# Kernel optimization log

Measured on AMD Instinct MI355X. Metric: run time of the kernel, lower is better.

## Reference

```python
import jax, jax.numpy as jnp
import numpy as np

DIM = 1024
DIM_HEAD = 64
HEADS = 16
DIM_INNER = DIM_HEAD * HEADS  # 1024


def setup_inputs() -> dict:
    key = jax.random.key(0)
    k1, k2, k3 = jax.random.split(key, 3)
    b, n = 2, 2048
    x = jax.random.normal(k1, (b, n, DIM), dtype=jnp.float32)
    gamma = jnp.ones((DIM,), dtype=jnp.float32)
    # torch Linear weight [out,in] applied as x @ W.T; store pre-transposed [in,out]
    w_qkv = jax.random.normal(k2, (DIM, 3 * DIM_INNER), dtype=jnp.float32) * (DIM ** -0.5)
    w_out = jax.random.normal(k3, (DIM_INNER, DIM), dtype=jnp.float32) * (DIM_INNER ** -0.5)
    return {"x": x, "gamma": gamma, "w_qkv": w_qkv, "w_out": w_out}


def reference(x, gamma, w_qkv, w_out):
    h, d = HEADS, DIM_HEAD
    scale = d ** -0.5
    rms_scale = DIM ** 0.5
    # RMSNorm: F.normalize(x, dim=-1) * sqrt(dim) * gamma  (eps=1e-12 clamp on L2 norm)
    norm = jnp.maximum(jnp.linalg.norm(x, axis=-1, keepdims=True), 1e-12)
    xn = x / norm * rms_scale * gamma
    b, n, _ = x.shape
    qkv = xn @ w_qkv  # [b, n, 3*h*d]
    qkv = qkv.reshape(b, n, 3, h, d)
    q = qkv[:, :, 0].transpose(0, 2, 1, 3) * scale  # [b, h, n, d]
    k = qkv[:, :, 1].transpose(0, 2, 1, 3)
    v = qkv[:, :, 2].transpose(0, 2, 1, 3)
    sim = jnp.einsum('bhid,bhjd->bhij', q, k)  # [b, h, n, n]
    causal_mask = jnp.triu(jnp.ones((n, n), dtype=bool), k=1)
    neg = -jnp.finfo(sim.dtype).max
    sim = jnp.where(causal_mask, neg, sim)
    attn = jax.nn.softmax(sim, axis=-1)
    out = jnp.einsum('bhij,bhjd->bhid', attn, v)  # [b, h, n, d]
    out = out.transpose(0, 2, 1, 3).reshape(b, n, h * d)
    return out @ w_out
```

## Files before the change

### kernel.cpp

```cpp
#include <hip/hip_runtime.h>
#include <hip/hip_bf16.h>

typedef __bf16 bf16x8 __attribute__((ext_vector_type(8)));
typedef short s16x4 __attribute__((ext_vector_type(4)));
typedef short s16x8 __attribute__((ext_vector_type(8)));
typedef float f32x4 __attribute__((ext_vector_type(4)));
typedef unsigned short u16x8 __attribute__((ext_vector_type(8)));

#define MFMA_K32(a, b, c) __builtin_amdgcn_mfma_f32_16x16x32_bf16(a, b, c, 0, 0, 0)

static __device__ __forceinline__ f32x4 mfma_k16(s16x4 a, s16x4 b, f32x4 c) {
#ifdef __HIP_DEVICE_COMPILE__
    return __builtin_amdgcn_mfma_f32_16x16x16bf16_1k(a, b, c, 0, 0, 0);
#else
    return c;
#endif
}

static __device__ __forceinline__ float fast_exp2(float x) {
#ifdef __HIP_DEVICE_COMPILE__
    return __builtin_amdgcn_exp2f(x);
#else
    return x;
#endif
}

#define GLL16(gp, lp)                                              \
    __builtin_amdgcn_global_load_lds(                              \
        (const __attribute__((address_space(1))) void*)(gp),       \
        (__attribute__((address_space(3))) void*)(lp), 16, 0, 0)

static __device__ __forceinline__ unsigned short f2bf(float f) {
    unsigned int u = __float_as_uint(f);
    u += 0x7fffu + ((u >> 16) & 1u);
    return (unsigned short)(u >> 16);
}

static __device__ __forceinline__ unsigned int cvtpk_bf16(float lo, float hi) {
#if defined(__HIP_DEVICE_COMPILE__) && __has_builtin(__builtin_amdgcn_cvt_pk_bf16_f32)
    typedef __bf16 bf16x2 __attribute__((ext_vector_type(2)));
    bf16x2 r = __builtin_amdgcn_cvt_pk_bf16_f32(lo, hi);
    return __builtin_bit_cast(unsigned int, r);
#else
    return (unsigned int)f2bf(lo) | ((unsigned int)f2bf(hi) << 16);
#endif
}

#define LOG2E 1.44269504088896340736f

__global__ __launch_bounds__(256) void prep_k(
    const float* __restrict__ x, const float* __restrict__ gamma,
    const float* __restrict__ w_qkv, const float* __restrict__ w_out,
    unsigned short* __restrict__ xn, unsigned short* __restrict__ wtq,
    unsigned short* __restrict__ wto) {
    __shared__ float sm[32][33];
    int bid = blockIdx.x, tid = threadIdx.x;
    if (bid < 4096) {
        const float* in;
        unsigned short* out;
        int R = 1024, C, bx, by;
        if (bid < 3072) { in = w_qkv; out = wtq; C = 3072; bx = bid % 96; by = bid / 96; }
        else { int b2 = bid - 3072; in = w_out; out = wto; C = 1024; bx = b2 % 32; by = b2 / 32; }
        int c0 = bx * 32, r0 = by * 32;
        int tr = tid >> 5, tc = tid & 31;
#pragma unroll
        for (int i = 0; i < 4; i++)
            sm[tr + i * 8][tc] = in[(size_t)(r0 + tr + i * 8) * C + c0 + tc];
        __syncthreads();
#pragma unroll
        for (int i = 0; i < 4; i++)
            out[(size_t)(c0 + tr + i * 8) * R + r0 + tc] = f2bf(sm[tc][tr + i * 8]);
    } else {
        int row = bid - 4096;
        const float* xr = x + (size_t)row * 1024;
        float4 v = *(const float4*)(xr + tid * 4);
        float ss = v.x * v.x + v.y * v.y + v.z * v.z + v.w * v.w;
#pragma unroll
        for (int off = 1; off < 64; off <<= 1) ss += __shfl_xor(ss, off, 64);
        if ((tid & 63) == 0) sm[0][tid >> 6] = ss;
        __syncthreads();
        float tot = sm[0][0] + sm[0][1] + sm[0][2] + sm[0][3];
        float f = 32.0f / fmaxf(sqrtf(tot), 1e-12f);
        float4 g = *(const float4*)(gamma + tid * 4);
        uint2 o;
        o.x = cvtpk_bf16(v.x * f * g.x, v.y * f * g.y);
        o.y = cvtpk_bf16(v.z * f * g.z, v.w * f * g.w);
        *(uint2*)(xn + (size_t)row * 1024 + tid * 4) = o;
    }
}

template <int MODE, int BM>
__global__ __launch_bounds__(256) void gemm_bt_k(
    const unsigned short* __restrict__ A, const unsigned short* __restrict__ BT,
    float* __restrict__ C, unsigned short* __restrict__ qw,
    unsigned short* __restrict__ kw, unsigned short* __restrict__ vw,
    int M, int N, int K) {
    constexpr int RT = 4;
    constexpr int CT = (BM == 128) ? 4 : 2;
    __shared__ unsigned short As[BM][32];
    __shared__ unsigned short Bs[128][32];
    int tid = threadIdx.x;
    int wave = tid >> 6, lane = tid & 63, quad = lane >> 4, l16 = lane & 15;
    int wrb, wcb;
    if constexpr (BM == 128) { wrb = (wave >> 1) * 64; wcb = (wave & 1) * 64; }
    else { wrb = 0; wcb = wave * 32; }
    int m0 = blockIdx.y * BM, n0 = blockIdx.x * 128;
    int lrow = lane >> 2, lcol = (lane & 3) * 8;
    const unsigned short *Ag0, *Ag1 = nullptr;
    if constexpr (BM == 128) {
        Ag0 = A + (size_t)(m0 + wave * 32 + lrow) * K + lcol;
        Ag1 = A + (size_t)(m0 + wave * 32 + 16 + lrow) * K + lcol;
    } else {
        Ag0 = A + (size_t)(m0 + wave * 16 + lrow) * K + lcol;
    }
    const unsigned short* Bg0 = BT + (size_t)(n0 + wave * 32 + lrow) * K + lcol;
    const unsigned short* Bg1 = BT + (size_t)(n0 + wave * 32 + 16 + lrow) * K + lcol;
    f32x4 acc[RT][CT] = {};
    for (int k0 = 0; k0 < K; k0 += 32) {
        __syncthreads();
        if constexpr (BM == 128) {
            GLL16(Ag0 + k0, &As[wave * 32][0]);
            GLL16(Ag1 + k0, &As[wave * 32 + 16][0]);
        } else {
            GLL16(Ag0 + k0, &As[wave * 16][0]);
        }
        GLL16(Bg0 + k0, &Bs[wave * 32][0]);
        GLL16(Bg1 + k0, &Bs[wave * 32 + 16][0]);
        __syncthreads();
        bf16x8 af[RT], bfr[CT];
#pragma unroll
        for (int t = 0; t < RT; t++)
            af[t] = *(const bf16x8*)&As[wrb + t * 16 + l16][quad * 8];
#pragma unroll
        for (int t = 0; t < CT; t++)
            bfr[t] = *(const bf16x8*)&Bs[wcb + t * 16 + l16][quad * 8];
#pragma unroll
        for (int rt = 0; rt < RT; rt++)
#pragma unroll
            for (int ct = 0; ct < CT; ct++)
                acc[rt][ct] = MFMA_K32(af[rt], bfr[ct], acc[rt][ct]);
    }
#pragma unroll
    for (int rt = 0; rt < RT; rt++) {
        int mb = m0 + wrb + rt * 16 + quad * 4;
        int b = mb >> 11, nn = mb & 2047;
#pragma unroll
        for (int ct = 0; ct < CT; ct++) {
            int col = n0 + wcb + ct * 16 + l16;
            if (MODE == 0) {
#pragma unroll
                for (int r = 0; r < 4; r++)
                    C[(size_t)(mb + r) * N + col] = acc[rt][ct][r];
            } else {
                int sec = col >> 10, ci = col & 1023;
                int hh = ci >> 6, dd = ci & 63;
                int bh = b * 16 + hh;
                if (sec == 0) {
#pragma unroll
                    for (int r = 0; r < 4; r++)
                        qw[((size_t)bh * 2048 + nn + r) * 64 + dd] =
                            f2bf(acc[rt][ct][r] * (0.125f * LOG2E));
                } else if (sec == 1) {
#pragma unroll
                    for (int r = 0; r < 4; r++)
                        kw[((size_t)bh * 2048 + nn + r) * 64 + dd] = f2bf(acc[rt][ct][r]);
                } else {
                    uint2 pk;
                    pk.x = cvtpk_bf16(acc[rt][ct][0], acc[rt][ct][1]);
                    pk.y = cvtpk_bf16(acc[rt][ct][2], acc[rt][ct][3]);
                    int sb = (nn & ~63) | (((nn >> 2) & 3) << 4) | (((nn >> 4) & 3) << 2);
                    *(uint2*)&vw[((size_t)bh * 64 + dd) * 2048 + sb] = pk;
                }
            }
        }
    }
}

__global__ __launch_bounds__(256) void attn_k(
    const unsigned short* __restrict__ q, const unsigned short* __restrict__ k,
    const unsigned short* __restrict__ vt, unsigned short* __restrict__ o) {
    __shared__ unsigned short Ks[2][128][72];
    __shared__ unsigned short Vt[2][64][136];
    int bh = blockIdx.x;
    int qt = 31 - (int)blockIdx.y;
    int tid = threadIdx.x, wave = tid >> 6, lane = tid & 63;
    int quad = lane >> 4, l16 = lane & 15;
    int b = bh >> 4, h = bh & 15;
    const unsigned short* qg = q + (size_t)bh * 2048 * 64;
    const unsigned short* kg = k + (size_t)bh * 2048 * 64;
    const unsigned short* vg = vt + (size_t)bh * 64 * 2048;
    int krow = tid >> 1, kcol = (tid & 1) * 32;
    int vrow = tid >> 2, vcol = (tid & 3) * 32;
    int q0w = qt * 64 + wave * 16;
    bf16x8 bq[2];
#pragma unroll
    for (int ks = 0; ks < 2; ks++)
        bq[ks] = *(const bf16x8*)&qg[(size_t)(q0w + l16) * 64 + ks * 32 + quad * 8];
    f32x4 ot[4] = {};
    float mrun = -1e38f, lrun = 0.f;
    int nkt = (qt >> 1) + 1;
    u16x8 pk[4], pv[4];
    {
        const unsigned short* kp = kg + (size_t)krow * 64 + kcol;
        const unsigned short* vp = vg + (size_t)vrow * 2048 + vcol;
#pragma unroll
        for (int i = 0; i < 4; i++) {
            pk[i] = *(const u16x8*)(kp + i * 8);
            pv[i] = *(const u16x8*)(vp + i * 8);
        }
#pragma unroll
        for (int i = 0; i < 4; i++) {
            *(u16x8*)&Ks[0][krow][kcol + i * 8] = pk[i];
            *(u16x8*)&Vt[0][vrow][vcol + i * 8] = pv[i];
        }
    }
    __syncthreads();
    for (int kt = 0; kt < nkt; kt++) {
        int cb = kt & 1;
        bool pf = (kt + 1 < nkt);
        if (pf) {
            const unsigned short* kp = kg + (size_t)((kt + 1) * 128 + krow) * 64 + kcol;
            const unsigned short* vp = vg + (size_t)vrow * 2048 + (kt + 1) * 128 + vcol;
#pragma unroll
            for (int i = 0; i < 4; i++) {
                pk[i] = *(const u16x8*)(kp + i * 8);
                pv[i] = *(const u16x8*)(vp + i * 8);
            }
        }
        f32x4 sf[8];
#pragma unroll
        for (int ct = 0; ct < 8; ct++) {
            bf16x8 ak0 = *(const bf16x8*)&Ks[cb][ct * 16 + l16][quad * 8];
            bf16x8 ak1 = *(const bf16x8*)&Ks[cb][ct * 16 + l16][32 + quad * 8];
            f32x4 s = {};
            s = MFMA_K32(ak0, bq[0], s);
            s = MFMA_K32(ak1, bq[1], s);
            sf[ct] = s;
        }
        if (kt == nkt - 1) {
            int qrow = q0w + l16;
            int keyb = kt * 128 + quad * 4;
#pragma unroll
            for (int ct = 0; ct < 8; ct++)
#pragma unroll
                for (int r = 0; r < 4; r++)
                    if (keyb + ct * 16 + r > qrow) sf[ct][r] = -1e30f;
        }
        float mx = -1e30f;
#pragma unroll
        for (int ct = 0; ct < 8; ct++)
#pragma unroll
            for (int r = 0; r < 4; r++) mx = fmaxf(mx, sf[ct][r]);
        mx = fmaxf(mx, __shfl_xor(mx, 16, 64));
        mx = fmaxf(mx, __shfl_xor(mx, 32, 64));
        float mnew = fmaxf(mrun, mx);
        float al = fast_exp2(mrun - mnew);
        mrun = mnew;
        float rs = 0.f;
#pragma unroll
        for (int ct = 0; ct < 8; ct++)
#pragma unroll
            for (int r = 0; r < 4; r++) {
                float p = fast_exp2(sf[ct][r] - mnew);
                sf[ct][r] = p;
                rs += p;
            }
        rs += __shfl_xor(rs, 16, 64);
        rs += __shfl_xor(rs, 32, 64);
        lrun = lrun * al + rs;
        s16x4 bpr[8];
#pragma unroll
        for (int ct = 0; ct < 8; ct++) {
            uint2 u;
            u.x = cvtpk_bf16(sf[ct][0], sf[ct][1]);
            u.y = cvtpk_bf16(sf[ct][2], sf[ct][3]);
            bpr[ct] = __builtin_bit_cast(s16x4, u);
        }
        if (__any(al < 1.0f)) {
#pragma unroll
            for (int dt = 0; dt < 4; dt++)
#pragma unroll
                for (int r = 0; r < 4; r++) ot[dt][r] *= al;
        }
#pragma unroll
        for (int dt = 0; dt < 4; dt++) {
#pragma unroll
            for (int blk = 0; blk < 2; blk++)
#pragma unroll
                for (int p = 0; p < 2; p++) {
                    s16x8 av = *(const s16x8*)&Vt[cb][dt * 16 + l16]
                                                  [blk * 64 + quad * 16 + p * 8];
                    s16x4 lo = __builtin_shufflevector(av, av, 0, 1, 2, 3);
                    s16x4 hi = __builtin_shufflevector(av, av, 4, 5, 6, 7);
                    int ct = blk * 4 + p * 2;
                    ot[dt] = mfma_k16(lo, bpr[ct], ot[dt]);
                    ot[dt] = mfma_k16(hi, bpr[ct + 1], ot[dt]);
                }
        }
        if (pf) {
#pragma unroll
            for (int i = 0; i < 4; i++) {
                *(u16x8*)&Ks[1 - cb][krow][kcol + i * 8] = pk[i];
                *(u16x8*)&Vt[1 - cb][vrow][vcol + i * 8] = pv[i];
            }
        }
        __syncthreads();
    }
    float inv = 1.0f / lrun;
    size_t rowbase = ((size_t)b * 2048 + q0w + l16) * 1024 + h * 64;
#pragma unroll
    for (int dt = 0; dt < 4; dt++) {
        uint2 pk2;
        pk2.x = cvtpk_bf16(ot[dt][0] * inv, ot[dt][1] * inv);
        pk2.y = cvtpk_bf16(ot[dt][2] * inv, ot[dt][3] * inv);
        *(uint2*)&o[rowbase + dt * 16 + quad * 4] = pk2;
    }
}

extern "C" void kernel_launch(void* const* d_in, const int* in_sizes, int n_in,
                              void* d_out, int out_size, void* d_ws, size_t ws_size,
                              hipStream_t stream) {
    const float* x = (const float*)d_in[0];
    const float* gamma = (const float*)d_in[1];
    const float* w_qkv = (const float*)d_in[2];
    const float* w_out = (const float*)d_in[3];
    float* out = (float*)d_out;
    char* ws = (char*)d_ws;

    unsigned short* xn = (unsigned short*)(ws);
    unsigned short* wtq = (unsigned short*)(ws + 8388608);
    unsigned short* wto = (unsigned short*)(ws + 14680064);
    unsigned short* qw = (unsigned short*)(ws + 16777216);
    unsigned short* kw = (unsigned short*)(ws + 25165824);
    unsigned short* vw = (unsigned short*)(ws + 33554432);
    unsigned short* ao = xn;

    prep_k<<<8192, 256, 0, stream>>>(x, gamma, w_qkv, w_out, xn, wtq, wto);
    gemm_bt_k<1, 128><<<dim3(24, 32), 256, 0, stream>>>(xn, wtq, nullptr, qw, kw, vw,
                                                        4096, 3072, 1024);
    attn_k<<<dim3(32, 32), 256, 0, stream>>>(qw, kw, vw, ao);
    gemm_bt_k<0, 64><<<dim3(8, 64), 256, 0, stream>>>(ao, wto, out, nullptr, nullptr,
                                                      nullptr, 4096, 1024, 1024);
}
```

Baseline: 191.8 us.

## Process 128 queries per attention block and widen weight transpose tiles

The attention kernel now gives each block 128 query rows, so every wave handles two 16-row query slices. Each K/V tile loaded into shared memory is therefore reused for twice as many queries, and the grid has half as many blocks. The kernel gains a launch bound of 2 blocks per CU to keep registers in check, at the cost of more register state per thread. Separately, the weight transpose in the prep kernel now uses 32x128 tiles with float4 loads and packed ushort4 stores, which cuts the block count and makes memory accesses wider.

After: 199.2 us. 3.9% more time.

```diff
diff --git a/kernel.cpp b/kernel.cpp
--- a/kernel.cpp
+++ b/kernel.cpp
@@ -53,25 +53,33 @@
     const float* __restrict__ w_qkv, const float* __restrict__ w_out,
     unsigned short* __restrict__ xn, unsigned short* __restrict__ wtq,
     unsigned short* __restrict__ wto) {
-    __shared__ float sm[32][33];
+    __shared__ float sm[32][132];
     int bid = blockIdx.x, tid = threadIdx.x;
-    if (bid < 4096) {
+    if (bid < 1024) {
         const float* in;
         unsigned short* out;
         int R = 1024, C, bx, by;
-        if (bid < 3072) { in = w_qkv; out = wtq; C = 3072; bx = bid % 96; by = bid / 96; }
-        else { int b2 = bid - 3072; in = w_out; out = wto; C = 1024; bx = b2 % 32; by = b2 / 32; }
-        int c0 = bx * 32, r0 = by * 32;
-        int tr = tid >> 5, tc = tid & 31;
-#pragma unroll
-        for (int i = 0; i < 4; i++)
-            sm[tr + i * 8][tc] = in[(size_t)(r0 + tr + i * 8) * C + c0 + tc];
-        __syncthreads();
-#pragma unroll
-        for (int i = 0; i < 4; i++)
-            out[(size_t)(c0 + tr + i * 8) * R + r0 + tc] = f2bf(sm[tc][tr + i * 8]);
+        if (bid < 768) { in = w_qkv; out = wtq; C = 3072; bx = bid % 24; by = bid / 24; }
+        else { int b2 = bid - 768; in = w_out; out = wto; C = 1024; bx = b2 % 8; by = b2 / 8; }
+        int c0 = bx * 128, r0 = by * 32;
+        int row = tid >> 3, cb = (tid & 7) * 4;
+#pragma unroll
+        for (int j = 0; j < 4; j++)
+            *(float4*)&sm[row][cb + j * 32] =
+                *(const float4*)&in[(size_t)(r0 + row) * C + c0 + cb + j * 32];
+        __syncthreads();
+        int c = tid >> 1, hh = (tid & 1) * 16;
+#pragma unroll
+        for (int j = 0; j < 4; j++) {
+            ushort4 pk;
+            pk.x = f2bf(sm[hh + j * 4 + 0][c]);
+            pk.y = f2bf(sm[hh + j * 4 + 1][c]);
+            pk.z = f2bf(sm[hh + j * 4 + 2][c]);
+            pk.w = f2bf(sm[hh + j * 4 + 3][c]);
+            *(ushort4*)&out[(size_t)(c0 + c) * R + r0 + hh + j * 4] = pk;
+        }
     } else {
-        int row = bid - 4096;
+        int row = bid - 1024;
         const float* xr = x + (size_t)row * 1024;
         float4 v = *(const float4*)(xr + tid * 4);
         float ss = v.x * v.x + v.y * v.y + v.z * v.z + v.w * v.w;
@@ -176,13 +184,13 @@
     }
 }
 
-__global__ __launch_bounds__(256) void attn_k(
+__global__ __launch_bounds__(256, 2) void attn_k(
     const unsigned short* __restrict__ q, const unsigned short* __restrict__ k,
     const unsigned short* __restrict__ vt, unsigned short* __restrict__ o) {
     __shared__ unsigned short Ks[2][128][72];
     __shared__ unsigned short Vt[2][64][136];
     int bh = blockIdx.x;
-    int qt = 31 - (int)blockIdx.y;
+    int qb = 15 - (int)blockIdx.y;
     int tid = threadIdx.x, wave = tid >> 6, lane = tid & 63;
     int quad = lane >> 4, l16 = lane & 15;
     int b = bh >> 4, h = bh & 15;
@@ -191,14 +199,17 @@
     const unsigned short* vg = vt + (size_t)bh * 64 * 2048;
     int krow = tid >> 1, kcol = (tid & 1) * 32;
     int vrow = tid >> 2, vcol = (tid & 3) * 32;
-    int q0w = qt * 64 + wave * 16;
-    bf16x8 bq[2];
-#pragma unroll
-    for (int ks = 0; ks < 2; ks++)
-        bq[ks] = *(const bf16x8*)&qg[(size_t)(q0w + l16) * 64 + ks * 32 + quad * 8];
-    f32x4 ot[4] = {};
-    float mrun = -1e38f, lrun = 0.f;
-    int nkt = (qt >> 1) + 1;
+    int q0 = qb * 128;
+    bf16x8 bq[2][2];
+#pragma unroll
+    for (int s = 0; s < 2; s++)
+#pragma unroll
+        for (int ks = 0; ks < 2; ks++)
+            bq[s][ks] = *(const bf16x8*)&qg[(size_t)(q0 + s * 64 + wave * 16 + l16) * 64 +
+                                            ks * 32 + quad * 8];
+    f32x4 ot[2][4] = {};
+    float mrun[2] = {-1e38f, -1e38f}, lrun[2] = {0.f, 0.f};
+    int nkt = qb + 1;
     u16x8 pk[4], pv[4];
     {
         const unsigned short* kp = kg + (size_t)krow * 64 + kcol;
@@ -227,60 +238,70 @@
                 pv[i] = *(const u16x8*)(vp + i * 8);
             }
         }
-        f32x4 sf[8];
+        f32x4 sf[2][8];
 #pragma unroll
         for (int ct = 0; ct < 8; ct++) {
             bf16x8 ak0 = *(const bf16x8*)&Ks[cb][ct * 16 + l16][quad * 8];
             bf16x8 ak1 = *(const bf16x8*)&Ks[cb][ct * 16 + l16][32 + quad * 8];
-            f32x4 s = {};
-            s = MFMA_K32(ak0, bq[0], s);
-            s = MFMA_K32(ak1, bq[1], s);
-            sf[ct] = s;
+#pragma unroll
+            for (int s = 0; s < 2; s++) {
+                f32x4 t = {};
+                t = MFMA_K32(ak0, bq[s][0], t);
+                t = MFMA_K32(ak1, bq[s][1], t);
+                sf[s][ct] = t;
+            }
         }
         if (kt == nkt - 1) {
-            int qrow = q0w + l16;
             int keyb = kt * 128 + quad * 4;
 #pragma unroll
+            for (int s = 0; s < 2; s++) {
+                int qrow = q0 + s * 64 + wave * 16 + l16;
+#pragma unroll
+                for (int ct = 0; ct < 8; ct++)
+#pragma unroll
+                    for (int r = 0; r < 4; r++)
+                        if (keyb + ct * 16 + r > qrow) sf[s][ct][r] = -1e30f;
+            }
+        }
+        s16x4 bpr[2][8];
+        float al[2];
+#pragma unroll
+        for (int s = 0; s < 2; s++) {
+            float mx = -1e30f;
+#pragma unroll
             for (int ct = 0; ct < 8; ct++)
 #pragma unroll
-                for (int r = 0; r < 4; r++)
-                    if (keyb + ct * 16 + r > qrow) sf[ct][r] = -1e30f;
-        }
-        float mx = -1e30f;
-#pragma unroll
-        for (int ct = 0; ct < 8; ct++)
-#pragma unroll
-            for (int r = 0; r < 4; r++) mx = fmaxf(mx, sf[ct][r]);
-        mx = fmaxf(mx, __shfl_xor(mx, 16, 64));
-        mx = fmaxf(mx, __shfl_xor(mx, 32, 64));
-        float mnew = fmaxf(mrun, mx);
-        float al = fast_exp2(mrun - mnew);
-        mrun = mnew;
-        float rs = 0.f;
-#pragma unroll
-        for (int ct = 0; ct < 8; ct++)
-#pragma unroll
-            for (int r = 0; r < 4; r++) {
-                float p = fast_exp2(sf[ct][r] - mnew);
-                sf[ct][r] = p;
-                rs += p;
-            }
-        rs += __shfl_xor(rs, 16, 64);
-        rs += __shfl_xor(rs, 32, 64);
-        lrun = lrun * al + rs;
-        s16x4 bpr[8];
-#pragma unroll
-        for (int ct = 0; ct < 8; ct++) {
-            uint2 u;
-            u.x = cvtpk_bf16(sf[ct][0], sf[ct][1]);
-            u.y = cvtpk_bf16(sf[ct][2], sf[ct][3]);
-            bpr[ct] = __builtin_bit_cast(s16x4, u);
-        }
-        if (__any(al < 1.0f)) {
-#pragma unroll
-            for (int dt = 0; dt < 4; dt++)
-#pragma unroll
-                for (int r = 0; r < 4; r++) ot[dt][r] *= al;
+                for (int r = 0; r < 4; r++) mx = fmaxf(mx, sf[s][ct][r]);
+            mx = fmaxf(mx, __shfl_xor(mx, 16, 64));
+            mx = fmaxf(mx, __shfl_xor(mx, 32, 64));
+            float mnew = fmaxf(mrun[s], mx);
+            al[s] = fast_exp2(mrun[s] - mnew);
+            mrun[s] = mnew;
+            float rs = 0.f;
+#pragma unroll
+            for (int ct = 0; ct < 8; ct++)
+#pragma unroll
+                for (int r = 0; r < 4; r++) {
+                    float p = fast_exp2(sf[s][ct][r] - mnew);
+                    sf[s][ct][r] = p;
+                    rs += p;
+                }
+            rs += __shfl_xor(rs, 16, 64);
+            rs += __shfl_xor(rs, 32, 64);
+            lrun[s] = lrun[s] * al[s] + rs;
+#pragma unroll
+            for (int ct = 0; ct < 8; ct++) {
+                uint2 u;
+                u.x = cvtpk_bf16(sf[s][ct][0], sf[s][ct][1]);
+                u.y = cvtpk_bf16(sf[s][ct][2], sf[s][ct][3]);
+                bpr[s][ct] = __builtin_bit_cast(s16x4, u);
+            }
+            if (__any(al[s] < 1.0f)) {
+#pragma unroll
+                for (int dt = 0; dt < 4; dt++)
+#pragma unroll
+                    for (int r = 0; r < 4; r++) ot[s][dt][r] *= al[s];
+            }
         }
 #pragma unroll
         for (int dt = 0; dt < 4; dt++) {
@@ -293,8 +314,11 @@
                     s16x4 lo = __builtin_shufflevector(av, av, 0, 1, 2, 3);
                     s16x4 hi = __builtin_shufflevector(av, av, 4, 5, 6, 7);
                     int ct = blk * 4 + p * 2;
-                    ot[dt] = mfma_k16(lo, bpr[ct], ot[dt]);
-                    ot[dt] = mfma_k16(hi, bpr[ct + 1], ot[dt]);
+#pragma unroll
+                    for (int s = 0; s < 2; s++) {
+                        ot[s][dt] = mfma_k16(lo, bpr[s][ct], ot[s][dt]);
+                        ot[s][dt] = mfma_k16(hi, bpr[s][ct + 1], ot[s][dt]);
+                    }
                 }
         }
         if (pf) {
@@ -306,14 +330,17 @@
         }
         __syncthreads();
     }
-    float inv = 1.0f / lrun;
-    size_t rowbase = ((size_t)b * 2048 + q0w + l16) * 1024 + h * 64;
-#pragma unroll
-    for (int dt = 0; dt < 4; dt++) {
-        uint2 pk2;
-        pk2.x = cvtpk_bf16(ot[dt][0] * inv, ot[dt][1] * inv);
-        pk2.y = cvtpk_bf16(ot[dt][2] * inv, ot[dt][3] * inv);
-        *(uint2*)&o[rowbase + dt * 16 + quad * 4] = pk2;
+#pragma unroll
+    for (int s = 0; s < 2; s++) {
+        float inv = 1.0f / lrun[s];
+        size_t rowbase = ((size_t)b * 2048 + q0 + s * 64 + wave * 16 + l16) * 1024 + h * 64;
+#pragma unroll
+        for (int dt = 0; dt < 4; dt++) {
+            uint2 pk2;
+            pk2.x = cvtpk_bf16(ot[s][dt][0] * inv, ot[s][dt][1] * inv);
+            pk2.y = cvtpk_bf16(ot[s][dt][2] * inv, ot[s][dt][3] * inv);
+            *(uint2*)&o[rowbase + dt * 16 + quad * 4] = pk2;
+        }
     }
 }
 
@@ -335,10 +362,10 @@
     unsigned short* vw = (unsigned short*)(ws + 33554432);
     unsigned short* ao = xn;
 
-    prep_k<<<8192, 256, 0, stream>>>(x, gamma, w_qkv, w_out, xn, wtq, wto);
+    prep_k<<<5120, 256, 0, stream>>>(x, gamma, w_qkv, w_out, xn, wtq, wto);
     gemm_bt_k<1, 128><<<dim3(24, 32), 256, 0, stream>>>(xn, wtq, nullptr, qw, kw, vw,
                                                         4096, 3072, 1024);
-    attn_k<<<dim3(32, 32), 256, 0, stream>>>(qw, kw, vw, ao);
+    attn_k<<<dim3(32, 16), 256, 0, stream>>>(qw, kw, vw, ao);
     gemm_bt_k<0, 64><<<dim3(8, 64), 256, 0, stream>>>(ao, wto, out, nullptr, nullptr,
                                                       nullptr, 4096, 1024, 1024);
 }
```

## Persistent atomic work queue for attention and transposed QKV GEMM epilogue

Applied to the files above, without the earlier changes.

The attention kernel becomes a persistent kernel of 512 blocks. Each block pulls (query-tile, head) work items from a global atomic counter, heaviest causal tiles first, which is meant to even out the triangular load imbalance and reduce tail idle time. Launch bounds now request two blocks per CU. The QKV GEMM swaps its operands so the output is computed transposed, letting Q and K be written as packed 8-byte stores instead of scalar bf16 stores. V stores become scalar strided writes in exchange, and a memset plus an atomic are added per launch.

New measurement: 194.8 us. Within noise of the previous version (+1.6%).

```diff
diff --git a/kernel.cpp b/kernel.cpp
--- a/kernel.cpp
+++ b/kernel.cpp
@@ -143,7 +143,6 @@
 #pragma unroll
     for (int rt = 0; rt < RT; rt++) {
         int mb = m0 + wrb + rt * 16 + quad * 4;
-        int b = mb >> 11, nn = mb & 2047;
 #pragma unroll
         for (int ct = 0; ct < CT; ct++) {
             int col = n0 + wcb + ct * 16 + l16;
@@ -152,168 +151,181 @@
                 for (int r = 0; r < 4; r++)
                     C[(size_t)(mb + r) * N + col] = acc[rt][ct][r];
             } else {
-                int sec = col >> 10, ci = col & 1023;
-                int hh = ci >> 6, dd = ci & 63;
-                int bh = b * 16 + hh;
+                int sec = mb >> 10, ci = mb & 1023;
+                int hh = ci >> 6, ddb = ci & 63;
+                int bb = col >> 11, t = col & 2047;
+                int bh = bb * 16 + hh;
                 if (sec == 0) {
-#pragma unroll
-                    for (int r = 0; r < 4; r++)
-                        qw[((size_t)bh * 2048 + nn + r) * 64 + dd] =
-                            f2bf(acc[rt][ct][r] * (0.125f * LOG2E));
+                    uint2 pk;
+                    pk.x = cvtpk_bf16(acc[rt][ct][0] * (0.125f * LOG2E),
+                                      acc[rt][ct][1] * (0.125f * LOG2E));
+                    pk.y = cvtpk_bf16(acc[rt][ct][2] * (0.125f * LOG2E),
+                                      acc[rt][ct][3] * (0.125f * LOG2E));
+                    *(uint2*)&qw[((size_t)bh * 2048 + t) * 64 + ddb] = pk;
                 } else if (sec == 1) {
-#pragma unroll
-                    for (int r = 0; r < 4; r++)
-                        kw[((size_t)bh * 2048 + nn + r) * 64 + dd] = f2bf(acc[rt][ct][r]);
-                } else {
                     uint2 pk;
                     pk.x = cvtpk_bf16(acc[rt][ct][0], acc[rt][ct][1]);
                     pk.y = cvtpk_bf16(acc[rt][ct][2], acc[rt][ct][3]);
-                    int sb = (nn & ~63) | (((nn >> 2) & 3) << 4) | (((nn >> 4) & 3) << 2);
-                    *(uint2*)&vw[((size_t)bh * 64 + dd) * 2048 + sb] = pk;
+                    *(uint2*)&kw[((size_t)bh * 2048 + t) * 64 + ddb] = pk;
+                } else {
+                    int sb = (t & ~63) | (((t >> 2) & 3) << 4) |
+                             (((t >> 4) & 3) << 2) | (t & 3);
+#pragma unroll
+                    for (int r = 0; r < 4; r++)
+                        vw[((size_t)bh * 64 + ddb + r) * 2048 + sb] =
+                            f2bf(acc[rt][ct][r]);
                 }
             }
         }
     }
 }
 
-__global__ __launch_bounds__(256) void attn_k(
+__global__ __launch_bounds__(256, 2) void attn_k(
     const unsigned short* __restrict__ q, const unsigned short* __restrict__ k,
-    const unsigned short* __restrict__ vt, unsigned short* __restrict__ o) {
+    const unsigned short* __restrict__ vt, unsigned short* __restrict__ o,
+    int* __restrict__ counter) {
     __shared__ unsigned short Ks[2][128][72];
     __shared__ unsigned short Vt[2][64][136];
-    int bh = blockIdx.x;
-    int qt = 31 - (int)blockIdx.y;
+    __shared__ int item_sh;
     int tid = threadIdx.x, wave = tid >> 6, lane = tid & 63;
     int quad = lane >> 4, l16 = lane & 15;
-    int b = bh >> 4, h = bh & 15;
-    const unsigned short* qg = q + (size_t)bh * 2048 * 64;
-    const unsigned short* kg = k + (size_t)bh * 2048 * 64;
-    const unsigned short* vg = vt + (size_t)bh * 64 * 2048;
     int krow = tid >> 1, kcol = (tid & 1) * 32;
     int vrow = tid >> 2, vcol = (tid & 3) * 32;
-    int q0w = qt * 64 + wave * 16;
-    bf16x8 bq[2];
-#pragma unroll
-    for (int ks = 0; ks < 2; ks++)
-        bq[ks] = *(const bf16x8*)&qg[(size_t)(q0w + l16) * 64 + ks * 32 + quad * 8];
-    f32x4 ot[4] = {};
-    float mrun = -1e38f, lrun = 0.f;
-    int nkt = (qt >> 1) + 1;
-    u16x8 pk[4], pv[4];
-    {
-        const unsigned short* kp = kg + (size_t)krow * 64 + kcol;
-        const unsigned short* vp = vg + (size_t)vrow * 2048 + vcol;
-#pragma unroll
-        for (int i = 0; i < 4; i++) {
-            pk[i] = *(const u16x8*)(kp + i * 8);
-            pv[i] = *(const u16x8*)(vp + i * 8);
-        }
-#pragma unroll
-        for (int i = 0; i < 4; i++) {
-            *(u16x8*)&Ks[0][krow][kcol + i * 8] = pk[i];
-            *(u16x8*)&Vt[0][vrow][vcol + i * 8] = pv[i];
-        }
-    }
-    __syncthreads();
-    for (int kt = 0; kt < nkt; kt++) {
-        int cb = kt & 1;
-        bool pf = (kt + 1 < nkt);
-        if (pf) {
-            const unsigned short* kp = kg + (size_t)((kt + 1) * 128 + krow) * 64 + kcol;
-            const unsigned short* vp = vg + (size_t)vrow * 2048 + (kt + 1) * 128 + vcol;
+    for (;;) {
+        if (tid == 0) item_sh = atomicAdd(counter, 1);
+        __syncthreads();
+        int item = item_sh;
+        if (item >= 1024) break;
+        int qt = 31 - (item >> 5);
+        int bh = item & 31;
+        int b = bh >> 4, h = bh & 15;
+        const unsigned short* qg = q + (size_t)bh * 2048 * 64;
+        const unsigned short* kg = k + (size_t)bh * 2048 * 64;
+        const unsigned short* vg = vt + (size_t)bh * 64 * 2048;
+        int q0w = qt * 64 + wave * 16;
+        bf16x8 bq[2];
+#pragma unroll
+        for (int ks = 0; ks < 2; ks++)
+            bq[ks] = *(const bf16x8*)&qg[(size_t)(q0w + l16) * 64 + ks * 32 + quad * 8];
+        f32x4 ot[4] = {};
+        float mrun = -1e38f, lrun = 0.f;
+        int nkt = (qt >> 1) + 1;
+        u16x8 pk[4], pv[4];
+        {
+            const unsigned short* kp = kg + (size_t)krow * 64 + kcol;
+            const unsigned short* vp = vg + (size_t)vrow * 2048 + vcol;
 #pragma unroll
             for (int i = 0; i < 4; i++) {
                 pk[i] = *(const u16x8*)(kp + i * 8);
                 pv[i] = *(const u16x8*)(vp + i * 8);
             }
-        }
-        f32x4 sf[8];
-#pragma unroll
-        for (int ct = 0; ct < 8; ct++) {
-            bf16x8 ak0 = *(const bf16x8*)&Ks[cb][ct * 16 + l16][quad * 8];
-            bf16x8 ak1 = *(const bf16x8*)&Ks[cb][ct * 16 + l16][32 + quad * 8];
-            f32x4 s = {};
-            s = MFMA_K32(ak0, bq[0], s);
-            s = MFMA_K32(ak1, bq[1], s);
-            sf[ct] = s;
-        }
-        if (kt == nkt - 1) {
-            int qrow = q0w + l16;
-            int keyb = kt * 128 + quad * 4;
+#pragma unroll
+            for (int i = 0; i < 4; i++) {
+                *(u16x8*)&Ks[0][krow][kcol + i * 8] = pk[i];
+                *(u16x8*)&Vt[0][vrow][vcol + i * 8] = pv[i];
+            }
+        }
+        __syncthreads();
+        for (int kt = 0; kt < nkt; kt++) {
+            int cb = kt & 1;
+            bool pf = (kt + 1 < nkt);
+            if (pf) {
+                const unsigned short* kp = kg + (size_t)((kt + 1) * 128 + krow) * 64 + kcol;
+                const unsigned short* vp = vg + (size_t)vrow * 2048 + (kt + 1) * 128 + vcol;
+#pragma unroll
+                for (int i = 0; i < 4; i++) {
+                    pk[i] = *(const u16x8*)(kp + i * 8);
+                    pv[i] = *(const u16x8*)(vp + i * 8);
+                }
+            }
+            f32x4 sf[8];
+#pragma unroll
+            for (int ct = 0; ct < 8; ct++) {
+                bf16x8 ak0 = *(const bf16x8*)&Ks[cb][ct * 16 + l16][quad * 8];
+                bf16x8 ak1 = *(const bf16x8*)&Ks[cb][ct * 16 + l16][32 + quad * 8];
+                f32x4 s = {};
+                s = MFMA_K32(ak0, bq[0], s);
+                s = MFMA_K32(ak1, bq[1], s);
+                sf[ct] = s;
+            }
+            if (kt == nkt - 1) {
+                int qrow = q0w + l16;
+                int keyb = kt * 128 + quad * 4;
+#pragma unroll
+                for (int ct = 0; ct < 8; ct++)
+#pragma unroll
+                    for (int r = 0; r < 4; r++)
+                        if (keyb + ct * 16 + r > qrow) sf[ct][r] = -1e30f;
+            }
+            float mx = -1e30f;
 #pragma unroll
             for (int ct = 0; ct < 8; ct++)
 #pragma unroll
-                for (int r = 0; r < 4; r++)
-                    if (keyb + ct * 16 + r > qrow) sf[ct][r] = -1e30f;
-        }
-        float mx = -1e30f;
-#pragma unroll
-        for (int ct = 0; ct < 8; ct++)
-#pragma unroll
-            for (int r = 0; r < 4; r++) mx = fmaxf(mx, sf[ct][r]);
-        mx = fmaxf(mx, __shfl_xor(mx, 16, 64));
-        mx = fmaxf(mx, __shfl_xor(mx, 32, 64));
-        float mnew = fmaxf(mrun, mx);
-        float al = fast_exp2(mrun - mnew);
-        mrun = mnew;
-        float rs = 0.f;
-#pragma unroll
-        for (int ct = 0; ct < 8; ct++)
-#pragma unroll
-            for (int r = 0; r < 4; r++) {
-                float p = fast_exp2(sf[ct][r] - mnew);
-                sf[ct][r] = p;
-                rs += p;
-            }
-        rs += __shfl_xor(rs, 16, 64);
-        rs += __shfl_xor(rs, 32, 64);
-        lrun = lrun * al + rs;
-        s16x4 bpr[8];
-#pragma unroll
-        for (int ct = 0; ct < 8; ct++) {
-            uint2 u;
-            u.x = cvtpk_bf16(sf[ct][0], sf[ct][1]);
-            u.y = cvtpk_bf16(sf[ct][2], sf[ct][3]);
-            bpr[ct] = __builtin_bit_cast(s16x4, u);
-        }
-        if (__any(al < 1.0f)) {
-#pragma unroll
-            for (int dt = 0; dt < 4; dt++)
-#pragma unroll
-                for (int r = 0; r < 4; r++) ot[dt][r] *= al;
-        }
+                for (int r = 0; r < 4; r++) mx = fmaxf(mx, sf[ct][r]);
+            mx = fmaxf(mx, __shfl_xor(mx, 16, 64));
+            mx = fmaxf(mx, __shfl_xor(mx, 32, 64));
+            float mnew = fmaxf(mrun, mx);
+            float al = fast_exp2(mrun - mnew);
+            mrun = mnew;
+            float rs = 0.f;
+#pragma unroll
+            for (int ct = 0; ct < 8; ct++)
+#pragma unroll
+                for (int r = 0; r < 4; r++) {
+                    float p = fast_exp2(sf[ct][r] - mnew);
+                    sf[ct][r] = p;
+                    rs += p;
+                }
+            rs += __shfl_xor(rs, 16, 64);
+            rs += __shfl_xor(rs, 32, 64);
+            lrun = lrun * al + rs;
+            s16x4 bpr[8];
+#pragma unroll
+            for (int ct = 0; ct < 8; ct++) {
+                uint2 u;
+                u.x = cvtpk_bf16(sf[ct][0], sf[ct][1]);
+                u.y = cvtpk_bf16(sf[ct][2], sf[ct][3]);
+                bpr[ct] = __builtin_bit_cast(s16x4, u);
+            }
+            if (__any(al < 1.0f)) {
+#pragma unroll
+                for (int dt = 0; dt < 4; dt++)
+#pragma unroll
+                    for (int r = 0; r < 4; r++) ot[dt][r] *= al;
+            }
+#pragma unroll
+            for (int dt = 0; dt < 4; dt++) {
+#pragma unroll
+                for (int blk = 0; blk < 2; blk++)
+#pragma unroll
+                    for (int p = 0; p < 2; p++) {
+                        s16x8 av = *(const s16x8*)&Vt[cb][dt * 16 + l16]
+                                                      [blk * 64 + quad * 16 + p * 8];
+                        s16x4 lo = __builtin_shufflevector(av, av, 0, 1, 2, 3);
+                        s16x4 hi = __builtin_shufflevector(av, av, 4, 5, 6, 7);
+                        int ct = blk * 4 + p * 2;
+                        ot[dt] = mfma_k16(lo, bpr[ct], ot[dt]);
+                        ot[dt] = mfma_k16(hi, bpr[ct + 1], ot[dt]);
+                    }
+            }
+            if (pf) {
+#pragma unroll
+                for (int i = 0; i < 4; i++) {
+                    *(u16x8*)&Ks[1 - cb][krow][kcol + i * 8] = pk[i];
+                    *(u16x8*)&Vt[1 - cb][vrow][vcol + i * 8] = pv[i];
+                }
+            }
+            __syncthreads();
+        }
+        float inv = 1.0f / lrun;
+        size_t rowbase = ((size_t)b * 2048 + q0w + l16) * 1024 + h * 64;
 #pragma unroll
         for (int dt = 0; dt < 4; dt++) {
-#pragma unroll
-            for (int blk = 0; blk < 2; blk++)
-#pragma unroll
-                for (int p = 0; p < 2; p++) {
-                    s16x8 av = *(const s16x8*)&Vt[cb][dt * 16 + l16]
-                                                  [blk * 64 + quad * 16 + p * 8];
-                    s16x4 lo = __builtin_shufflevector(av, av, 0, 1, 2, 3);
-                    s16x4 hi = __builtin_shufflevector(av, av, 4, 5, 6, 7);
-                    int ct = blk * 4 + p * 2;
-                    ot[dt] = mfma_k16(lo, bpr[ct], ot[dt]);
-                    ot[dt] = mfma_k16(hi, bpr[ct + 1], ot[dt]);
-                }
-        }
-        if (pf) {
-#pragma unroll
-            for (int i = 0; i < 4; i++) {
-                *(u16x8*)&Ks[1 - cb][krow][kcol + i * 8] = pk[i];
-                *(u16x8*)&Vt[1 - cb][vrow][vcol + i * 8] = pv[i];
-            }
-        }
-        __syncthreads();
-    }
-    float inv = 1.0f / lrun;
-    size_t rowbase = ((size_t)b * 2048 + q0w + l16) * 1024 + h * 64;
-#pragma unroll
-    for (int dt = 0; dt < 4; dt++) {
-        uint2 pk2;
-        pk2.x = cvtpk_bf16(ot[dt][0] * inv, ot[dt][1] * inv);
-        pk2.y = cvtpk_bf16(ot[dt][2] * inv, ot[dt][3] * inv);
-        *(uint2*)&o[rowbase + dt * 16 + quad * 4] = pk2;
+            uint2 pk2;
+            pk2.x = cvtpk_bf16(ot[dt][0] * inv, ot[dt][1] * inv);
+            pk2.y = cvtpk_bf16(ot[dt][2] * inv, ot[dt][3] * inv);
+            *(uint2*)&o[rowbase + dt * 16 + quad * 4] = pk2;
+        }
     }
 }
 
@@ -334,11 +346,13 @@
     unsigned short* kw = (unsigned short*)(ws + 25165824);
     unsigned short* vw = (unsigned short*)(ws + 33554432);
     unsigned short* ao = xn;
+    int* counter = (int*)(ws + 8388608);
 
     prep_k<<<8192, 256, 0, stream>>>(x, gamma, w_qkv, w_out, xn, wtq, wto);
-    gemm_bt_k<1, 128><<<dim3(24, 32), 256, 0, stream>>>(xn, wtq, nullptr, qw, kw, vw,
-                                                        4096, 3072, 1024);
-    attn_k<<<dim3(32, 32), 256, 0, stream>>>(qw, kw, vw, ao);
+    gemm_bt_k<2, 128><<<dim3(32, 24), 256, 0, stream>>>(wtq, xn, nullptr, qw, kw, vw,
+                                                        3072, 4096, 1024);
+    hipMemsetAsync(counter, 0, 4, stream);
+    attn_k<<<512, 256, 0, stream>>>(qw, kw, vw, ao, counter);
     gemm_bt_k<0, 64><<<dim3(8, 64), 256, 0, stream>>>(ao, wto, out, nullptr, nullptr,
                                                       nullptr, 4096, 1024, 1024);
 }
```
